# Kernel optimization log

Hardware: AMD Instinct MI355X
Metric: run time of the kernel (lower is better)

The kernel has to match this reference:

```python
import jax, jax.numpy as jnp
import numpy as np

T, D = 4096, 1024
S = 32768
DIST_DIM = 20
BINS = jnp.array([1, 2, 3, 4, 8, 16, 32, 64], dtype=jnp.int64)


def setup_inputs() -> dict:
    key = jax.random.key(0)
    ks = jax.random.split(key, 16)
    scale = 1.0 / np.sqrt(D)
    inp = {
        "embeds": jax.random.normal(ks[0], (T, D), dtype=jnp.float32),
        "states": jax.random.normal(ks[1], (T, D), dtype=jnp.float32),
        # MHA (1 head) projection params, torch Linear convention: x @ W.T + b
        "Wq": jax.random.normal(ks[2], (D, D), dtype=jnp.float32) * scale,
        "bq": jnp.zeros((D,), dtype=jnp.float32),
        "Wk": jax.random.normal(ks[3], (D, D), dtype=jnp.float32) * scale,
        "bk": jnp.zeros((D,), dtype=jnp.float32),
        "Wv": jax.random.normal(ks[4], (D, D), dtype=jnp.float32) * scale,
        "bv": jnp.zeros((D,), dtype=jnp.float32),
        "Wo": jax.random.normal(ks[5], (D, D), dtype=jnp.float32) * scale,
        "bo": jnp.zeros((D,), dtype=jnp.float32),
        # distance embedding table: len(bins)+1 = 9 rows
        "dist_embed": jax.random.normal(ks[6], (9, DIST_DIM), dtype=jnp.float32),
        "span_starts": jax.random.randint(ks[7], (S,), 0, T - 30, dtype=jnp.int64),
        "span_lengths": jax.random.randint(ks[8], (S,), 0, 30, dtype=jnp.int64),
    }
    return inp


def reference(embeds, states, Wq, bq, Wk, bk, Wv, bv, Wo, bo, dist_embed,
              span_starts, span_lengths):
    d = states.shape[1]
    # Single-head attention: query=states, key=states, value=embeds (seq len T, batch 1)
    q = states @ Wq.T + bq                      # [T, D]
    k = states @ Wk.T + bk                      # [T, D]
    v = embeds @ Wv.T + bv                      # [T, D]
    scores = (q @ k.T) / jnp.sqrt(jnp.asarray(d, q.dtype))   # [T, T]
    attn = jax.nn.softmax(scores, axis=-1)
    attn_embeds = (attn @ v) @ Wo.T + bo        # [T, D]

    ends = span_starts + span_lengths           # inclusive end, width 1..30
    # ragged per-span segment sum over [start, end] via prefix sums
    cs = jnp.concatenate([jnp.zeros((1, d), attn_embeds.dtype),
                          jnp.cumsum(attn_embeds, axis=0)], axis=0)  # [T+1, D]
    span_sum = cs[ends + 1] - cs[span_starts]   # [S, D]

    span_start_end = jnp.concatenate([states[span_starts], states[ends]], axis=1)  # [S, 2D]

    lengths = span_lengths + 1                  # len(span) = end - start + 1
    bin_idx = jnp.sum(lengths[:, None] > BINS[None, :], axis=-1)  # [S] in [0, 8]
    len_embed = dist_embed[bin_idx]             # [S, DIST_DIM] (dropout omitted: eval mode)

    return jnp.concatenate([span_sum, span_start_end, len_embed], axis=1)  # [S, 3D+20]
```

## Files before the change

### kernel.cpp

```cpp
#include <hip/hip_runtime.h>
#include <hip/hip_bf16.h>


typedef __attribute__((ext_vector_type(8))) short bf16x8;
typedef __attribute__((ext_vector_type(4))) short bf16x4;
typedef __attribute__((ext_vector_type(4))) float f32x4;

#define T_DIM 4096
#define D_DIM 1024
#define S_NUM 32768

#define GLOBAL_LOAD_LDS16(gptr, ldsptr)                                        \
  __builtin_amdgcn_global_load_lds(                                            \
      (const __attribute__((address_space(1))) void*)(gptr),                   \
      (__attribute__((address_space(3))) void*)(ldsptr), 16, 0, 0)

__global__ __launch_bounds__(256) void cast2_bf16(const float* __restrict__ a,
                                                  const float* __restrict__ b,
                                                  __hip_bfloat16* __restrict__ oa,
                                                  __hip_bfloat16* __restrict__ ob) {
  const float* s = blockIdx.z ? b : a;
  __hip_bfloat16* d = blockIdx.z ? ob : oa;
  int i = blockIdx.x * 256 + threadIdx.x;
  float2 v = ((const float2*)s)[i];
  __hip_bfloat162 o;
  o.x = __float2bfloat16(v.x);
  o.y = __float2bfloat16(v.y);
  ((__hip_bfloat162*)d)[i] = o;
}

__global__ __launch_bounds__(256) void cast3_bf16(const float* __restrict__ a,
                                                  const float* __restrict__ b,
                                                  const float* __restrict__ c,
                                                  __hip_bfloat16* __restrict__ oa,
                                                  __hip_bfloat16* __restrict__ ob,
                                                  __hip_bfloat16* __restrict__ oc) {
  const int z = blockIdx.z;
  const float* s = z == 0 ? a : z == 1 ? b : c;
  __hip_bfloat16* d = z == 0 ? oa : z == 1 ? ob : oc;
  int i = blockIdx.x * 256 + threadIdx.x;
  float2 v = ((const float2*)s)[i];
  __hip_bfloat162 o;
  o.x = __float2bfloat16(v.x);
  o.y = __float2bfloat16(v.y);
  ((__hip_bfloat162*)d)[i] = o;
}

__global__ __launch_bounds__(256) void transpose_cast_bf16(const float* __restrict__ in,
                                                           __hip_bfloat16* __restrict__ out) {
  __shared__ float tile[64][65];
  const int bx = blockIdx.x * 64;
  const int by = blockIdx.y * 64;
  const int t = threadIdx.x;
  const int r = t >> 4;
  const int c4 = (t & 15) * 4;
#pragma unroll
  for (int p = 0; p < 4; p++) {
    const float4 v = *(const float4*)&in[(size_t)(by + p * 16 + r) * D_DIM + bx + c4];
    tile[p * 16 + r][c4] = v.x;
    tile[p * 16 + r][c4 + 1] = v.y;
    tile[p * 16 + r][c4 + 2] = v.z;
    tile[p * 16 + r][c4 + 3] = v.w;
  }
  __syncthreads();
#pragma unroll
  for (int p = 0; p < 4; p++) {
    const int orow = p * 16 + r;
    bf16x4 o4;
#pragma unroll
    for (int q = 0; q < 4; q++) {
      __hip_bfloat16 h = __float2bfloat16(tile[c4 + q][orow]);
      o4[q] = *reinterpret_cast<short*>(&h);
    }
    *reinterpret_cast<bf16x4*>(&out[(size_t)(bx + orow) * D_DIM + by + c4]) = o4;
  }
}

__global__ __launch_bounds__(256) void zero_f32(float* __restrict__ p, int n) {
  int i = blockIdx.x * 256 + threadIdx.x;
  if (i < n) p[i] = 0.0f;
}

__global__ __launch_bounds__(256) void bias_fuse(const float* __restrict__ Wo,
                                                 const float* __restrict__ bv,
                                                 const float* __restrict__ bo,
                                                 float* __restrict__ bvo) {
  const int wave = threadIdx.x >> 6, lane = threadIdx.x & 63;
  const int row = blockIdx.x * 4 + wave;
  float s = 0.0f;
  for (int k = lane; k < D_DIM; k += 64) s += Wo[(size_t)row * D_DIM + k] * bv[k];
#pragma unroll
  for (int off = 32; off; off >>= 1) s += __shfl_xor(s, off);
  if (lane == 0) bvo[row] = s + bo[row];
}

__device__ __forceinline__ void gemm_core_128(const __hip_bfloat16* __restrict__ A,
                                              const __hip_bfloat16* __restrict__ B,
                                              int K, int lda, int ldb,
                                              int bm, int bn,
                                              __hip_bfloat16* As,
                                              __hip_bfloat16* Bs,
                                              f32x4 acc[4][4]) {
  const int tid = threadIdx.x;
  const int wave = tid >> 6, lane = tid & 63;
  const int srow = lane >> 2, scol = (lane & 3) * 8;
  const __hip_bfloat16* Ag0 = A + (size_t)(bm + wave * 16 + srow) * lda + scol;
  const __hip_bfloat16* Ag1 = Ag0 + (size_t)64 * lda;
  const __hip_bfloat16* Bg0 = B + (size_t)(bn + wave * 16 + srow) * ldb + scol;
  const __hip_bfloat16* Bg1 = Bg0 + (size_t)64 * ldb;
  const int c0 = wave * 512, c1 = (4 + wave) * 512;
  const int wtr = (wave >> 1) * 64, wtc = (wave & 1) * 64;
  const int lr = lane & 15, lk = (lane >> 4) * 8;

  GLOBAL_LOAD_LDS16(Ag0, As + c0);
  GLOBAL_LOAD_LDS16(Ag1, As + c1);
  GLOBAL_LOAD_LDS16(Bg0, Bs + c0);
  GLOBAL_LOAD_LDS16(Bg1, Bs + c1);

  int cur = 0;
  for (int k0 = 0; k0 < K; k0 += 32) {
    __syncthreads();
    const int nxt = cur ^ 1;
    if (k0 + 32 < K) {
      const int kn = k0 + 32;
      GLOBAL_LOAD_LDS16(Ag0 + kn, As + nxt * 4096 + c0);
      GLOBAL_LOAD_LDS16(Ag1 + kn, As + nxt * 4096 + c1);
      GLOBAL_LOAD_LDS16(Bg0 + kn, Bs + nxt * 4096 + c0);
      GLOBAL_LOAD_LDS16(Bg1 + kn, Bs + nxt * 4096 + c1);
    }
    const __hip_bfloat16* a = As + cur * 4096;
    const __hip_bfloat16* b = Bs + cur * 4096;
    bf16x8 af[4], bfr[4];
#pragma unroll
    for (int i = 0; i < 4; i++)
      af[i] = *(const bf16x8*)&a[(wtr + i * 16 + lr) * 32 + lk];
#pragma unroll
    for (int j = 0; j < 4; j++)
      bfr[j] = *(const bf16x8*)&b[(wtc + j * 16 + lr) * 32 + lk];
#pragma unroll
    for (int i = 0; i < 4; i++)
#pragma unroll
      for (int j = 0; j < 4; j++)
        acc[i][j] = __builtin_amdgcn_mfma_f32_16x16x32_bf16(af[i], bfr[j], acc[i][j], 0, 0, 0);
    cur = nxt;
  }
}


__global__ __launch_bounds__(256) void wvo_gemm_splitk(const __hip_bfloat16* __restrict__ Wo_bf,
                                                       const __hip_bfloat16* __restrict__ WvT_bf,
                                                       float* __restrict__ part) {
  __shared__ __hip_bfloat16 As[2 * 128 * 32];
  __shared__ __hip_bfloat16 Bs[2 * 128 * 32];
  const int z = blockIdx.z;
  const int bm = blockIdx.y * 128, bn = blockIdx.x * 128;
  const int wave = threadIdx.x >> 6, lane = threadIdx.x & 63;
  const int wtr = (wave >> 1) * 64, wtc = (wave & 1) * 64;
  const int lr = lane & 15;
  f32x4 acc[4][4] = {};
  gemm_core_128(Wo_bf + z * 256, WvT_bf + z * 256, 256, D_DIM, D_DIM, bm, bn, As, Bs, acc);
  float* dst = part + (size_t)z * D_DIM * D_DIM;
#pragma unroll
  for (int j = 0; j < 4; j++) {
    const int col = bn + wtc + j * 16 + lr;
#pragma unroll
    for (int i = 0; i < 4; i++)
#pragma unroll
      for (int r = 0; r < 4; r++) {
        const int row = bm + wtr + i * 16 + (lane >> 4) * 4 + r;
        dst[(size_t)row * D_DIM + col] = acc[i][j][r];
      }
  }
}

__global__ __launch_bounds__(256) void wvo_combine(const float* __restrict__ part,
                                                   __hip_bfloat16* __restrict__ out) {
  const size_t idx = (size_t)blockIdx.x * 256 + threadIdx.x;
  const size_t n = (size_t)D_DIM * D_DIM / 4;
  f32x4 s = ((const f32x4*)part)[idx];
  s += ((const f32x4*)part)[idx + n];
  s += ((const f32x4*)part)[idx + 2 * n];
  s += ((const f32x4*)part)[idx + 3 * n];
  bf16x4 o;
#pragma unroll
  for (int q = 0; q < 4; q++) {
    __hip_bfloat16 h = __float2bfloat16(s[q]);
    o[q] = *reinterpret_cast<short*>(&h);
  }
  ((bf16x4*)out)[idx] = o;
}

__global__ __launch_bounds__(256) void qkv_gemm(const __hip_bfloat16* __restrict__ states_bf,
                                                const __hip_bfloat16* __restrict__ embeds_bf,
                                                const __hip_bfloat16* __restrict__ Wq,
                                                const __hip_bfloat16* __restrict__ Wk,
                                                const __hip_bfloat16* __restrict__ Wvo,
                                                const float* __restrict__ bq,
                                                const float* __restrict__ bk,
                                                __hip_bfloat16* __restrict__ q,
                                                __hip_bfloat16* __restrict__ k,
                                                __hip_bfloat16* __restrict__ vT) {
  __shared__ __hip_bfloat16 As[2 * 128 * 32];
  __shared__ __hip_bfloat16 Bs[2 * 128 * 32];
  const int z = blockIdx.z;
  const __hip_bfloat16* A = (z == 2) ? embeds_bf : states_bf;
  const __hip_bfloat16* B = (z == 0) ? Wq : (z == 1) ? Wk : Wvo;
  const float* bias = (z == 0) ? bq : bk;
  const int bm = blockIdx.y * 128, bn = blockIdx.x * 128;
  const int wave = threadIdx.x >> 6, lane = threadIdx.x & 63;
  const int wtr = (wave >> 1) * 64, wtc = (wave & 1) * 64;
  const int lr = lane & 15;
  f32x4 acc[4][4] = {};
  gemm_core_128(A, B, D_DIM, D_DIM, D_DIM, bm, bn, As, Bs, acc);

#pragma unroll
  for (int j = 0; j < 4; j++) {
    const int col = bn + wtc + j * 16 + lr;
    const float bb = (z == 2) ? 0.0f : bias[col];
#pragma unroll
    for (int i = 0; i < 4; i++) {
#pragma unroll
      for (int r = 0; r < 4; r++) {
        const int row = bm + wtr + i * 16 + (lane >> 4) * 4 + r;
        const __hip_bfloat16 val = __float2bfloat16(acc[i][j][r] + bb);
        if (z == 0)
          q[(size_t)row * D_DIM + col] = val;
        else if (z == 1)
          k[(size_t)row * D_DIM + col] = val;
        else
          vT[(size_t)col * T_DIM + row] = val;
      }
    }
  }
}

__global__ __launch_bounds__(256) void scoresP_gemm(const __hip_bfloat16* __restrict__ q,
                                                    const __hip_bfloat16* __restrict__ k,
                                                    __hip_bfloat16* __restrict__ P,
                                                    float* __restrict__ l) {
  __shared__ __hip_bfloat16 As[2 * 128 * 32];
  __shared__ __hip_bfloat16 Bs[2 * 128 * 32];
  const int bm = blockIdx.y * 128, bn = blockIdx.x * 128;
  const int wave = threadIdx.x >> 6, lane = threadIdx.x & 63;
  const int wtr = (wave >> 1) * 64, wtc = (wave & 1) * 64;
  const int lr = lane & 15;
  f32x4 acc[4][4] = {};
  gemm_core_128(q, k, D_DIM, D_DIM, D_DIM, bm, bn, As, Bs, acc);

  float rowsum[4][4];
#pragma unroll
  for (int i = 0; i < 4; i++)
#pragma unroll
    for (int r = 0; r < 4; r++) rowsum[i][r] = 0.0f;

#pragma unroll
  for (int j = 0; j < 4; j++) {
    const int col = bn + wtc + j * 16 + lr;
#pragma unroll
    for (int i = 0; i < 4; i++) {
#pragma unroll
      for (int r = 0; r < 4; r++) {
        const int row = bm + wtr + i * 16 + (lane >> 4) * 4 + r;
        const float e = __expf(acc[i][j][r] * 0.03125f);
        P[(size_t)row * T_DIM + col] = __float2bfloat16(e);
        rowsum[i][r] += e;
      }
    }
  }
#pragma unroll
  for (int off = 1; off < 16; off <<= 1)
#pragma unroll
    for (int i = 0; i < 4; i++)
#pragma unroll
      for (int r = 0; r < 4; r++)
        rowsum[i][r] += __shfl_xor(rowsum[i][r], off);
  if ((lane & 15) == 0) {
#pragma unroll
    for (int i = 0; i < 4; i++)
#pragma unroll
      for (int r = 0; r < 4; r++) {
        const int row = bm + wtr + i * 16 + (lane >> 4) * 4 + r;
        atomicAdd(&l[row], rowsum[i][r]);
      }
  }
}

__global__ __launch_bounds__(256) void pv_gemm_splitk(const __hip_bfloat16* __restrict__ P,
                                                      const __hip_bfloat16* __restrict__ vT,
                                                      float* __restrict__ part) {
  __shared__ __hip_bfloat16 As[2 * 128 * 32];
  __shared__ __hip_bfloat16 Bs[2 * 128 * 32];
  const int z = blockIdx.z;
  const int bm = blockIdx.y * 128, bn = blockIdx.x * 128;
  const int wave = threadIdx.x >> 6, lane = threadIdx.x & 63;
  const int wtr = (wave >> 1) * 64, wtc = (wave & 1) * 64;
  const int lr = lane & 15;
  f32x4 acc[4][4] = {};
  gemm_core_128(P + z * 2048, vT + z * 2048, 2048, T_DIM, T_DIM, bm, bn, As, Bs, acc);
  float* dst = part + (size_t)z * T_DIM * D_DIM;
#pragma unroll
  for (int j = 0; j < 4; j++) {
    const int col = bn + wtc + j * 16 + lr;
#pragma unroll
    for (int i = 0; i < 4; i++)
#pragma unroll
      for (int r = 0; r < 4; r++) {
        const int row = bm + wtr + i * 16 + (lane >> 4) * 4 + r;
        dst[(size_t)row * D_DIM + col] = acc[i][j][r];
      }
  }
}

__global__ __launch_bounds__(256) void pv_combine(const float* __restrict__ part,
                                                  const float* __restrict__ l,
                                                  const float* __restrict__ bvo,
                                                  float* __restrict__ ao) {
  const size_t idx = (size_t)blockIdx.x * 256 + threadIdx.x;
  const size_t n = (size_t)T_DIM * D_DIM / 4;
  const int row = (int)(idx >> 8);
  const int c4 = (int)(idx & 255) * 4;
  const float inv = 1.0f / l[row];
  f32x4 a = ((const f32x4*)part)[idx];
  f32x4 b = ((const f32x4*)part)[idx + n];
  f32x4 bb = *(const f32x4*)(bvo + c4);
  f32x4 r = (a + b) * inv + bb;
  ((f32x4*)ao)[idx] = r;
}

__global__ __launch_bounds__(256) void colsum_chunks(const float* __restrict__ x,
                                                     float* __restrict__ part) {
  const int col = blockIdx.x * 256 + threadIdx.x;
  const int ch = blockIdx.y;
  const float* p = x + (size_t)ch * 64 * D_DIM + col;
  float s = 0.0f;
#pragma unroll 8
  for (int i = 0; i < 64; i++) s += p[i * D_DIM];
  part[ch * D_DIM + col] = s;
}

__global__ __launch_bounds__(256) void scan_chunks(float* part) {
  const int col = blockIdx.x * 256 + threadIdx.x;
  float run = 0.0f;
  for (int ch = 0; ch < 64; ch++) {
    const float t = part[ch * D_DIM + col];
    part[ch * D_DIM + col] = run;
    run += t;
  }
}

__global__ __launch_bounds__(256) void write_cs(const float* __restrict__ x,
                                                const float* __restrict__ part,
                                                float* __restrict__ cs) {
  const int col = blockIdx.x * 256 + threadIdx.x;
  const int ch = blockIdx.y;
  float run = part[ch * D_DIM + col];
  if (ch == 0) cs[col] = 0.0f;
  const float* p = x + (size_t)ch * 64 * D_DIM + col;
  float* q = cs + ((size_t)(ch * 64 + 1)) * D_DIM + col;
  for (int i = 0; i < 64; i++) {
    run += p[i * D_DIM];
    q[i * D_DIM] = run;
  }
}

__global__ __launch_bounds__(256) void hist_k(const int* __restrict__ starts,
                                              int* __restrict__ hist) {
  const int s = blockIdx.x * 256 + threadIdx.x;
  atomicAdd(&hist[starts[s]], 1);
}

__global__ __launch_bounds__(1024) void scan_hist(const int* __restrict__ hist,
                                                  int* __restrict__ offs) {
  __shared__ int sums[1024];
  const int t = threadIdx.x;
  const int v0 = hist[t * 4], v1 = hist[t * 4 + 1];
  const int v2 = hist[t * 4 + 2], v3 = hist[t * 4 + 3];
  const int tot = v0 + v1 + v2 + v3;
  sums[t] = tot;
  __syncthreads();
  for (int off = 1; off < 1024; off <<= 1) {
    const int x = (t >= off) ? sums[t - off] : 0;
    __syncthreads();
    sums[t] += x;
    __syncthreads();
  }
  const int excl = sums[t] - tot;
  offs[t * 4] = excl;
  offs[t * 4 + 1] = excl + v0;
  offs[t * 4 + 2] = excl + v0 + v1;
  offs[t * 4 + 3] = excl + v0 + v1 + v2;
}

__global__ __launch_bounds__(256) void scatter_k(const int* __restrict__ starts,
                                                 int* __restrict__ offs,
                                                 int* __restrict__ perm) {
  const int s = blockIdx.x * 256 + threadIdx.x;
  const int pos = atomicAdd(&offs[starts[s]], 1);
  perm[pos] = s;
}

__global__ __launch_bounds__(256) void span_gather(const float* __restrict__ cs,
                                                   const float* __restrict__ states,
                                                   const float* __restrict__ dist,
                                                   const int* __restrict__ starts,
                                                   const int* __restrict__ lens,
                                                   const int* __restrict__ perm,
                                                   float* __restrict__ out) {
  const int s = perm[blockIdx.x];
  const int start = starts[s];
  const int len = lens[s];
  const int end = start + len;
  const int length = len + 1;
  const int bin = (length > 1) + (length > 2) + (length > 3) + (length > 4) +
                  (length > 8) + (length > 16) + (length > 32) + (length > 64);
  const f32x4* csS = (const f32x4*)(cs + (size_t)start * D_DIM);
  const f32x4* csE = (const f32x4*)(cs + (size_t)(end + 1) * D_DIM);
  const f32x4* stS = (const f32x4*)(states + (size_t)start * D_DIM);
  const f32x4* stE = (const f32x4*)(states + (size_t)end * D_DIM);
  const f32x4* de = (const f32x4*)(dist + bin * 20);
  f32x4* o = (f32x4*)(out + (size_t)s * 3092);
  for (int j = threadIdx.x; j < 773; j += 256) {
    f32x4 r;
    if (j < 256) {
      r = csE[j] - csS[j];
    } else if (j < 512) {
      r = stS[j - 256];
    } else if (j < 768) {
      r = stE[j - 512];
    } else {
      r = de[j - 768];
    }
    __builtin_nontemporal_store(r, o + j);
  }
}

extern "C" void kernel_launch(void* const* d_in, const int* in_sizes, int n_in,
                              void* d_out, int out_size, void* d_ws, size_t ws_size,
                              hipStream_t stream) {
  const float* embeds = (const float*)d_in[0];
  const float* states = (const float*)d_in[1];
  const float* Wq = (const float*)d_in[2];
  const float* bq = (const float*)d_in[3];
  const float* Wk = (const float*)d_in[4];
  const float* bk = (const float*)d_in[5];
  const float* Wv = (const float*)d_in[6];
  const float* bv = (const float*)d_in[7];
  const float* Wo = (const float*)d_in[8];
  const float* bo = (const float*)d_in[9];
  const float* dist = (const float*)d_in[10];
  const int* starts = (const int*)d_in[11];
  const int* lens = (const int*)d_in[12];
  float* out = (float*)d_out;

  const size_t TD = (size_t)T_DIM * D_DIM;
  const size_t DD = (size_t)D_DIM * D_DIM;
  const size_t TT = (size_t)T_DIM * T_DIM;

  char* w = (char*)d_ws;
  size_t off = 0;
  auto alloc = [&](size_t bytes) {
    char* p = w + off;
    off = (off + bytes + 255) & ~(size_t)255;
    return p;
  };
  __hip_bfloat16* states_bf = (__hip_bfloat16*)alloc(TD * 2);
  __hip_bfloat16* embeds_bf = (__hip_bfloat16*)alloc(TD * 2);
  __hip_bfloat16* Wq_bf = (__hip_bfloat16*)alloc(DD * 2);
  __hip_bfloat16* Wk_bf = (__hip_bfloat16*)alloc(DD * 2);
  __hip_bfloat16* Wo_bf = (__hip_bfloat16*)alloc(DD * 2);
  __hip_bfloat16* WvT_bf = (__hip_bfloat16*)alloc(DD * 2);
  __hip_bfloat16* Wvo_bf = (__hip_bfloat16*)alloc(DD * 2);
  __hip_bfloat16* q_bf = (__hip_bfloat16*)alloc(TD * 2);
  __hip_bfloat16* k_bf = (__hip_bfloat16*)alloc(TD * 2);
  __hip_bfloat16* vT_bf = (__hip_bfloat16*)alloc(TD * 2);
  __hip_bfloat16* P_bf = (__hip_bfloat16*)alloc(TT * 2);
  float* l_sum = (float*)alloc(T_DIM * 4);
  int* hist = (int*)alloc(T_DIM * 4);
  int* offs = (int*)alloc(T_DIM * 4);
  int* perm = (int*)alloc(S_NUM * 4);
  float* bvo = (float*)alloc(D_DIM * 4);
  float* ao = (float*)alloc(TD * 4);
  float* cs = (float*)alloc((size_t)(T_DIM + 1) * D_DIM * 4);
  float* part = (float*)alloc(64 * D_DIM * 4);
  float* wvo_part = (float*)alloc(4 * DD * 4);
  float* pv_part = (float*)alloc(2 * TD * 4);
  if (off > ws_size) return;

  cast2_bf16<<<dim3(TD / 512, 1, 2), 256, 0, stream>>>(states, embeds, states_bf, embeds_bf);
  cast3_bf16<<<dim3(DD / 512, 1, 3), 256, 0, stream>>>(Wq, Wk, Wo, Wq_bf, Wk_bf, Wo_bf);
  transpose_cast_bf16<<<dim3(16, 16), 256, 0, stream>>>(Wv, WvT_bf);
  zero_f32<<<2 * T_DIM / 256, 256, 0, stream>>>(l_sum, 2 * T_DIM);
  bias_fuse<<<D_DIM / 4, 256, 0, stream>>>(Wo, bv, bo, bvo);

  hist_k<<<S_NUM / 256, 256, 0, stream>>>(starts, hist);
  scan_hist<<<1, 1024, 0, stream>>>(hist, offs);
  scatter_k<<<S_NUM / 256, 256, 0, stream>>>(starts, offs, perm);

  wvo_gemm_splitk<<<dim3(D_DIM / 128, D_DIM / 128, 4), 256, 0, stream>>>(Wo_bf, WvT_bf, wvo_part);
  wvo_combine<<<DD / 1024, 256, 0, stream>>>(wvo_part, Wvo_bf);

  qkv_gemm<<<dim3(D_DIM / 128, T_DIM / 128, 3), 256, 0, stream>>>(
      states_bf, embeds_bf, Wq_bf, Wk_bf, Wvo_bf, bq, bk, q_bf, k_bf, vT_bf);

  scoresP_gemm<<<dim3(T_DIM / 128, T_DIM / 128), 256, 0, stream>>>(q_bf, k_bf, P_bf, l_sum);

  pv_gemm_splitk<<<dim3(D_DIM / 128, T_DIM / 128, 2), 256, 0, stream>>>(P_bf, vT_bf, pv_part);
  pv_combine<<<TD / 1024, 256, 0, stream>>>(pv_part, l_sum, bvo, ao);

  colsum_chunks<<<dim3(4, 64), 256, 0, stream>>>(ao, part);
  scan_chunks<<<4, 256, 0, stream>>>(part);
  write_cs<<<dim3(4, 64), 256, 0, stream>>>(ao, part, cs);

  span_gather<<<S_NUM, 256, 0, stream>>>(cs, states, dist, starts, lens, perm, out);
}
```

Measured before the change: 712.0 us.

## Fold Wq·Wk into one weight product and fuse PV combine with column sums

Scores are rewritten as states·(Wq^T Wk)·states^T plus bias-derived row and column vectors. The Q and K projection GEMMs (two T×D×D) become one small D×D×D weight GEMM plus one T×D×D projection GEMM, so projection work is roughly halved. The PV combine is also fused with the per-chunk column sums, and the separate chunk-scan kernel is removed. Each write_cs block now rescans the partial sums itself. Precision differs because the combined weight M1 is rounded to bf16 and the raw states replace the rounded q and k.

```diff
diff --git a/kernel.cpp b/kernel.cpp
--- a/kernel.cpp
+++ b/kernel.cpp
@@ -29,26 +29,26 @@
   ((__hip_bfloat162*)d)[i] = o;
 }
 
-__global__ __launch_bounds__(256) void cast3_bf16(const float* __restrict__ a,
-                                                  const float* __restrict__ b,
-                                                  const float* __restrict__ c,
-                                                  __hip_bfloat16* __restrict__ oa,
-                                                  __hip_bfloat16* __restrict__ ob,
-                                                  __hip_bfloat16* __restrict__ oc) {
-  const int z = blockIdx.z;
-  const float* s = z == 0 ? a : z == 1 ? b : c;
-  __hip_bfloat16* d = z == 0 ? oa : z == 1 ? ob : oc;
+__global__ __launch_bounds__(256) void cast1_bf16(const float* __restrict__ a,
+                                                  __hip_bfloat16* __restrict__ oa) {
   int i = blockIdx.x * 256 + threadIdx.x;
-  float2 v = ((const float2*)s)[i];
+  float2 v = ((const float2*)a)[i];
   __hip_bfloat162 o;
   o.x = __float2bfloat16(v.x);
   o.y = __float2bfloat16(v.y);
-  ((__hip_bfloat162*)d)[i] = o;
-}
-
-__global__ __launch_bounds__(256) void transpose_cast_bf16(const float* __restrict__ in,
-                                                           __hip_bfloat16* __restrict__ out) {
+  ((__hip_bfloat162*)oa)[i] = o;
+}
+
+__global__ __launch_bounds__(256) void transpose_cast_bf16(const float* __restrict__ wq,
+                                                           const float* __restrict__ wk,
+                                                           const float* __restrict__ wv,
+                                                           __hip_bfloat16* __restrict__ oq,
+                                                           __hip_bfloat16* __restrict__ ok,
+                                                           __hip_bfloat16* __restrict__ ov) {
   __shared__ float tile[64][65];
+  const int z = blockIdx.z;
+  const float* in = z == 0 ? wq : z == 1 ? wk : wv;
+  __hip_bfloat16* out = z == 0 ? oq : z == 1 ? ok : ov;
   const int bx = blockIdx.x * 64;
   const int by = blockIdx.y * 64;
   const int t = threadIdx.x;
@@ -81,17 +81,61 @@
   if (i < n) p[i] = 0.0f;
 }
 
-__global__ __launch_bounds__(256) void bias_fuse(const float* __restrict__ Wo,
-                                                 const float* __restrict__ bv,
-                                                 const float* __restrict__ bo,
-                                                 float* __restrict__ bvo) {
+__global__ __launch_bounds__(256) void hvec(const float* __restrict__ Wo,
+                                            const float* __restrict__ bv,
+                                            const float* __restrict__ bo,
+                                            const __hip_bfloat16* __restrict__ WqT,
+                                            const __hip_bfloat16* __restrict__ WkT,
+                                            const float* __restrict__ bq,
+                                            const float* __restrict__ bk,
+                                            float* __restrict__ bvo,
+                                            float* __restrict__ h1,
+                                            float* __restrict__ h2,
+                                            float* __restrict__ c0) {
+  const int z = blockIdx.z;
   const int wave = threadIdx.x >> 6, lane = threadIdx.x & 63;
   const int row = blockIdx.x * 4 + wave;
+  if (z == 3 && (blockIdx.x != 0 || wave != 0)) return;
   float s = 0.0f;
-  for (int k = lane; k < D_DIM; k += 64) s += Wo[(size_t)row * D_DIM + k] * bv[k];
+  if (z == 0) {
+    for (int k2 = lane; k2 < D_DIM; k2 += 64) s += Wo[(size_t)row * D_DIM + k2] * bv[k2];
+  } else if (z == 1) {
+    for (int k2 = lane; k2 < D_DIM; k2 += 64)
+      s += __bfloat162float(WqT[(size_t)row * D_DIM + k2]) * bk[k2];
+  } else if (z == 2) {
+    for (int k2 = lane; k2 < D_DIM; k2 += 64)
+      s += __bfloat162float(WkT[(size_t)row * D_DIM + k2]) * bq[k2];
+  } else {
+    for (int k2 = lane; k2 < D_DIM; k2 += 64) s += bq[k2] * bk[k2];
+  }
 #pragma unroll
   for (int off = 32; off; off >>= 1) s += __shfl_xor(s, off);
-  if (lane == 0) bvo[row] = s + bo[row];
+  if (lane == 0) {
+    if (z == 0) bvo[row] = s + bo[row];
+    else if (z == 1) h1[row] = s;
+    else if (z == 2) h2[row] = s;
+    else c0[0] = s;
+  }
+}
+
+__global__ __launch_bounds__(256) void uw_vec(const float* __restrict__ states,
+                                              const float* __restrict__ h1,
+                                              const float* __restrict__ h2,
+                                              const float* __restrict__ c0,
+                                              float* __restrict__ u,
+                                              float* __restrict__ w) {
+  const int z = blockIdx.z;
+  const int wave = threadIdx.x >> 6, lane = threadIdx.x & 63;
+  const int row = blockIdx.x * 4 + wave;
+  const float* h = z == 0 ? h1 : h2;
+  float s = 0.0f;
+  for (int k2 = lane; k2 < D_DIM; k2 += 64) s += states[(size_t)row * D_DIM + k2] * h[k2];
+#pragma unroll
+  for (int off = 32; off; off >>= 1) s += __shfl_xor(s, off);
+  if (lane == 0) {
+    if (z == 0) u[row] = s + c0[0];
+    else w[row] = s;
+  }
 }
 
 __device__ __forceinline__ void gemm_core_128(const __hip_bfloat16* __restrict__ A,
@@ -147,18 +191,23 @@
 }
 
 
-__global__ __launch_bounds__(256) void wvo_gemm_splitk(const __hip_bfloat16* __restrict__ Wo_bf,
-                                                       const __hip_bfloat16* __restrict__ WvT_bf,
-                                                       float* __restrict__ part) {
+__global__ __launch_bounds__(256) void small_gemm_splitk(const __hip_bfloat16* __restrict__ Wo_bf,
+                                                         const __hip_bfloat16* __restrict__ WvT_bf,
+                                                         const __hip_bfloat16* __restrict__ WkT_bf,
+                                                         const __hip_bfloat16* __restrict__ WqT_bf,
+                                                         float* __restrict__ part) {
   __shared__ __hip_bfloat16 As[2 * 128 * 32];
   __shared__ __hip_bfloat16 Bs[2 * 128 * 32];
   const int z = blockIdx.z;
+  const int zz = z & 3;
+  const __hip_bfloat16* A = (z < 4) ? Wo_bf + zz * 256 : WkT_bf + zz * 256;
+  const __hip_bfloat16* B = (z < 4) ? WvT_bf + zz * 256 : WqT_bf + zz * 256;
   const int bm = blockIdx.y * 128, bn = blockIdx.x * 128;
   const int wave = threadIdx.x >> 6, lane = threadIdx.x & 63;
   const int wtr = (wave >> 1) * 64, wtc = (wave & 1) * 64;
   const int lr = lane & 15;
   f32x4 acc[4][4] = {};
-  gemm_core_128(Wo_bf + z * 256, WvT_bf + z * 256, 256, D_DIM, D_DIM, bm, bn, As, Bs, acc);
+  gemm_core_128(A, B, 256, D_DIM, D_DIM, bm, bn, As, Bs, acc);
   float* dst = part + (size_t)z * D_DIM * D_DIM;
 #pragma unroll
   for (int j = 0; j < 4; j++) {
@@ -173,39 +222,34 @@
   }
 }
 
-__global__ __launch_bounds__(256) void wvo_combine(const float* __restrict__ part,
-                                                   __hip_bfloat16* __restrict__ out) {
+__global__ __launch_bounds__(256) void small_combine(const float* __restrict__ part,
+                                                     __hip_bfloat16* __restrict__ wvo,
+                                                     __hip_bfloat16* __restrict__ m1) {
   const size_t idx = (size_t)blockIdx.x * 256 + threadIdx.x;
   const size_t n = (size_t)D_DIM * D_DIM / 4;
-  f32x4 s = ((const f32x4*)part)[idx];
-  s += ((const f32x4*)part)[idx + n];
-  s += ((const f32x4*)part)[idx + 2 * n];
-  s += ((const f32x4*)part)[idx + 3 * n];
+  const f32x4* base = (const f32x4*)part + (size_t)blockIdx.z * 4 * n;
+  f32x4 s = base[idx] + base[idx + n] + base[idx + 2 * n] + base[idx + 3 * n];
   bf16x4 o;
 #pragma unroll
   for (int q = 0; q < 4; q++) {
     __hip_bfloat16 h = __float2bfloat16(s[q]);
     o[q] = *reinterpret_cast<short*>(&h);
   }
+  __hip_bfloat16* out = blockIdx.z == 0 ? wvo : m1;
   ((bf16x4*)out)[idx] = o;
 }
 
-__global__ __launch_bounds__(256) void qkv_gemm(const __hip_bfloat16* __restrict__ states_bf,
-                                                const __hip_bfloat16* __restrict__ embeds_bf,
-                                                const __hip_bfloat16* __restrict__ Wq,
-                                                const __hip_bfloat16* __restrict__ Wk,
-                                                const __hip_bfloat16* __restrict__ Wvo,
-                                                const float* __restrict__ bq,
-                                                const float* __restrict__ bk,
-                                                __hip_bfloat16* __restrict__ q,
-                                                __hip_bfloat16* __restrict__ k,
-                                                __hip_bfloat16* __restrict__ vT) {
+__global__ __launch_bounds__(256) void proj_gemm(const __hip_bfloat16* __restrict__ states_bf,
+                                                 const __hip_bfloat16* __restrict__ embeds_bf,
+                                                 const __hip_bfloat16* __restrict__ M1,
+                                                 const __hip_bfloat16* __restrict__ Wvo,
+                                                 __hip_bfloat16* __restrict__ tmp,
+                                                 __hip_bfloat16* __restrict__ vT) {
   __shared__ __hip_bfloat16 As[2 * 128 * 32];
   __shared__ __hip_bfloat16 Bs[2 * 128 * 32];
   const int z = blockIdx.z;
-  const __hip_bfloat16* A = (z == 2) ? embeds_bf : states_bf;
-  const __hip_bfloat16* B = (z == 0) ? Wq : (z == 1) ? Wk : Wvo;
-  const float* bias = (z == 0) ? bq : bk;
+  const __hip_bfloat16* A = (z == 0) ? states_bf : embeds_bf;
+  const __hip_bfloat16* B = (z == 0) ? M1 : Wvo;
   const int bm = blockIdx.y * 128, bn = blockIdx.x * 128;
   const int wave = threadIdx.x >> 6, lane = threadIdx.x & 63;
   const int wtr = (wave >> 1) * 64, wtc = (wave & 1) * 64;
@@ -216,17 +260,14 @@
 #pragma unroll
   for (int j = 0; j < 4; j++) {
     const int col = bn + wtc + j * 16 + lr;
-    const float bb = (z == 2) ? 0.0f : bias[col];
 #pragma unroll
     for (int i = 0; i < 4; i++) {
 #pragma unroll
       for (int r = 0; r < 4; r++) {
         const int row = bm + wtr + i * 16 + (lane >> 4) * 4 + r;
-        const __hip_bfloat16 val = __float2bfloat16(acc[i][j][r] + bb);
+        const __hip_bfloat16 val = __float2bfloat16(acc[i][j][r]);
         if (z == 0)
-          q[(size_t)row * D_DIM + col] = val;
-        else if (z == 1)
-          k[(size_t)row * D_DIM + col] = val;
+          tmp[(size_t)row * D_DIM + col] = val;
         else
           vT[(size_t)col * T_DIM + row] = val;
       }
@@ -234,8 +275,10 @@
   }
 }
 
-__global__ __launch_bounds__(256) void scoresP_gemm(const __hip_bfloat16* __restrict__ q,
-                                                    const __hip_bfloat16* __restrict__ k,
+__global__ __launch_bounds__(256) void scoresP_gemm(const __hip_bfloat16* __restrict__ tmp,
+                                                    const __hip_bfloat16* __restrict__ states_bf,
+                                                    const float* __restrict__ u,
+                                                    const float* __restrict__ w,
                                                     __hip_bfloat16* __restrict__ P,
                                                     float* __restrict__ l) {
   __shared__ __hip_bfloat16 As[2 * 128 * 32];
@@ -245,7 +288,7 @@
   const int wtr = (wave >> 1) * 64, wtc = (wave & 1) * 64;
   const int lr = lane & 15;
   f32x4 acc[4][4] = {};
-  gemm_core_128(q, k, D_DIM, D_DIM, D_DIM, bm, bn, As, Bs, acc);
+  gemm_core_128(tmp, states_bf, D_DIM, D_DIM, D_DIM, bm, bn, As, Bs, acc);
 
   float rowsum[4][4];
 #pragma unroll
@@ -256,12 +299,13 @@
 #pragma unroll
   for (int j = 0; j < 4; j++) {
     const int col = bn + wtc + j * 16 + lr;
+    const float ww = w[col];
 #pragma unroll
     for (int i = 0; i < 4; i++) {
 #pragma unroll
       for (int r = 0; r < 4; r++) {
         const int row = bm + wtr + i * 16 + (lane >> 4) * 4 + r;
-        const float e = __expf(acc[i][j][r] * 0.03125f);
+        const float e = __expf((acc[i][j][r] + u[row] + ww) * 0.03125f);
         P[(size_t)row * T_DIM + col] = __float2bfloat16(e);
         rowsum[i][r] += e;
       }
@@ -311,49 +355,34 @@
   }
 }
 
-__global__ __launch_bounds__(256) void pv_combine(const float* __restrict__ part,
-                                                  const float* __restrict__ l,
-                                                  const float* __restrict__ bvo,
-                                                  float* __restrict__ ao) {
-  const size_t idx = (size_t)blockIdx.x * 256 + threadIdx.x;
-  const size_t n = (size_t)T_DIM * D_DIM / 4;
-  const int row = (int)(idx >> 8);
-  const int c4 = (int)(idx & 255) * 4;
-  const float inv = 1.0f / l[row];
-  f32x4 a = ((const f32x4*)part)[idx];
-  f32x4 b = ((const f32x4*)part)[idx + n];
-  f32x4 bb = *(const f32x4*)(bvo + c4);
-  f32x4 r = (a + b) * inv + bb;
-  ((f32x4*)ao)[idx] = r;
-}
-
-__global__ __launch_bounds__(256) void colsum_chunks(const float* __restrict__ x,
-                                                     float* __restrict__ part) {
+__global__ __launch_bounds__(256) void pv_combine_colsum(const float* __restrict__ part,
+                                                         const float* __restrict__ l,
+                                                         const float* __restrict__ bvo,
+                                                         float* __restrict__ ao,
+                                                         float* __restrict__ partT) {
   const int col = blockIdx.x * 256 + threadIdx.x;
   const int ch = blockIdx.y;
-  const float* p = x + (size_t)ch * 64 * D_DIM + col;
+  const size_t n = (size_t)T_DIM * D_DIM;
+  const float bb = bvo[col];
   float s = 0.0f;
-#pragma unroll 8
-  for (int i = 0; i < 64; i++) s += p[i * D_DIM];
-  part[ch * D_DIM + col] = s;
-}
-
-__global__ __launch_bounds__(256) void scan_chunks(float* part) {
-  const int col = blockIdx.x * 256 + threadIdx.x;
-  float run = 0.0f;
-  for (int ch = 0; ch < 64; ch++) {
-    const float t = part[ch * D_DIM + col];
-    part[ch * D_DIM + col] = run;
-    run += t;
-  }
+  for (int i = 0; i < 64; i++) {
+    const int row = ch * 64 + i;
+    const float inv = 1.0f / l[row];
+    const size_t idx = (size_t)row * D_DIM + col;
+    const float v = (part[idx] + part[n + idx]) * inv + bb;
+    ao[idx] = v;
+    s += v;
+  }
+  partT[(col << 6) | ch] = s;
 }
 
 __global__ __launch_bounds__(256) void write_cs(const float* __restrict__ x,
-                                                const float* __restrict__ part,
+                                                const float* __restrict__ partT,
                                                 float* __restrict__ cs) {
   const int col = blockIdx.x * 256 + threadIdx.x;
   const int ch = blockIdx.y;
-  float run = part[ch * D_DIM + col];
+  float run = 0.0f;
+  for (int c = 0; c < ch; c++) run += partT[(col << 6) | c];
   if (ch == 0) cs[col] = 0.0f;
   const float* p = x + (size_t)ch * 64 * D_DIM + col;
   float* q = cs + ((size_t)(ch * 64 + 1)) * D_DIM + col;
@@ -465,13 +494,13 @@
   };
   __hip_bfloat16* states_bf = (__hip_bfloat16*)alloc(TD * 2);
   __hip_bfloat16* embeds_bf = (__hip_bfloat16*)alloc(TD * 2);
-  __hip_bfloat16* Wq_bf = (__hip_bfloat16*)alloc(DD * 2);
-  __hip_bfloat16* Wk_bf = (__hip_bfloat16*)alloc(DD * 2);
   __hip_bfloat16* Wo_bf = (__hip_bfloat16*)alloc(DD * 2);
+  __hip_bfloat16* WqT_bf = (__hip_bfloat16*)alloc(DD * 2);
+  __hip_bfloat16* WkT_bf = (__hip_bfloat16*)alloc(DD * 2);
   __hip_bfloat16* WvT_bf = (__hip_bfloat16*)alloc(DD * 2);
   __hip_bfloat16* Wvo_bf = (__hip_bfloat16*)alloc(DD * 2);
-  __hip_bfloat16* q_bf = (__hip_bfloat16*)alloc(TD * 2);
-  __hip_bfloat16* k_bf = (__hip_bfloat16*)alloc(TD * 2);
+  __hip_bfloat16* M1_bf = (__hip_bfloat16*)alloc(DD * 2);
+  __hip_bfloat16* tmp_bf = (__hip_bfloat16*)alloc(TD * 2);
   __hip_bfloat16* vT_bf = (__hip_bfloat16*)alloc(TD * 2);
   __hip_bfloat16* P_bf = (__hip_bfloat16*)alloc(TT * 2);
   float* l_sum = (float*)alloc(T_DIM * 4);
@@ -479,37 +508,45 @@
   int* offs = (int*)alloc(T_DIM * 4);
   int* perm = (int*)alloc(S_NUM * 4);
   float* bvo = (float*)alloc(D_DIM * 4);
+  float* h1 = (float*)alloc(D_DIM * 4);
+  float* h2 = (float*)alloc(D_DIM * 4);
+  float* c0 = (float*)alloc(256);
+  float* u = (float*)alloc(T_DIM * 4);
+  float* wv_ = (float*)alloc(T_DIM * 4);
   float* ao = (float*)alloc(TD * 4);
   float* cs = (float*)alloc((size_t)(T_DIM + 1) * D_DIM * 4);
-  float* part = (float*)alloc(64 * D_DIM * 4);
-  float* wvo_part = (float*)alloc(4 * DD * 4);
+  float* partT = (float*)alloc(64 * D_DIM * 4);
+  float* wpart = (float*)alloc(8 * DD * 4);
   float* pv_part = (float*)alloc(2 * TD * 4);
   if (off > ws_size) return;
 
   cast2_bf16<<<dim3(TD / 512, 1, 2), 256, 0, stream>>>(states, embeds, states_bf, embeds_bf);
-  cast3_bf16<<<dim3(DD / 512, 1, 3), 256, 0, stream>>>(Wq, Wk, Wo, Wq_bf, Wk_bf, Wo_bf);
-  transpose_cast_bf16<<<dim3(16, 16), 256, 0, stream>>>(Wv, WvT_bf);
+  cast1_bf16<<<DD / 512, 256, 0, stream>>>(Wo, Wo_bf);
+  transpose_cast_bf16<<<dim3(16, 16, 3), 256, 0, stream>>>(Wq, Wk, Wv, WqT_bf, WkT_bf, WvT_bf);
   zero_f32<<<2 * T_DIM / 256, 256, 0, stream>>>(l_sum, 2 * T_DIM);
-  bias_fuse<<<D_DIM / 4, 256, 0, stream>>>(Wo, bv, bo, bvo);
+  hvec<<<dim3(D_DIM / 4, 1, 4), 256, 0, stream>>>(Wo, bv, bo, WqT_bf, WkT_bf, bq, bk,
+                                                  bvo, h1, h2, c0);
 
   hist_k<<<S_NUM / 256, 256, 0, stream>>>(starts, hist);
   scan_hist<<<1, 1024, 0, stream>>>(hist, offs);
   scatter_k<<<S_NUM / 256, 256, 0, stream>>>(starts, offs, perm);
 
-  wvo_gemm_splitk<<<dim3(D_DIM / 128, D_DIM / 128, 4), 256, 0, stream>>>(Wo_bf, WvT_bf, wvo_part);
-  wvo_combine<<<DD / 1024, 256, 0, stream>>>(wvo_part, Wvo_bf);
-
-  qkv_gemm<<<dim3(D_DIM / 128, T_DIM / 128, 3), 256, 0, stream>>>(
-      states_bf, embeds_bf, Wq_bf, Wk_bf, Wvo_bf, bq, bk, q_bf, k_bf, vT_bf);
-
-  scoresP_gemm<<<dim3(T_DIM / 128, T_DIM / 128), 256, 0, stream>>>(q_bf, k_bf, P_bf, l_sum);
+  uw_vec<<<dim3(T_DIM / 4, 1, 2), 256, 0, stream>>>(states, h1, h2, c0, u, wv_);
+
+  small_gemm_splitk<<<dim3(D_DIM / 128, D_DIM / 128, 8), 256, 0, stream>>>(
+      Wo_bf, WvT_bf, WkT_bf, WqT_bf, wpart);
+  small_combine<<<dim3(DD / 1024, 1, 2), 256, 0, stream>>>(wpart, Wvo_bf, M1_bf);
+
+  proj_gemm<<<dim3(D_DIM / 128, T_DIM / 128, 2), 256, 0, stream>>>(
+      states_bf, embeds_bf, M1_bf, Wvo_bf, tmp_bf, vT_bf);
+
+  scoresP_gemm<<<dim3(T_DIM / 128, T_DIM / 128), 256, 0, stream>>>(
+      tmp_bf, states_bf, u, wv_, P_bf, l_sum);
 
   pv_gemm_splitk<<<dim3(D_DIM / 128, T_DIM / 128, 2), 256, 0, stream>>>(P_bf, vT_bf, pv_part);
-  pv_combine<<<TD / 1024, 256, 0, stream>>>(pv_part, l_sum, bvo, ao);
-
-  colsum_chunks<<<dim3(4, 64), 256, 0, stream>>>(ao, part);
-  scan_chunks<<<4, 256, 0, stream>>>(part);
-  write_cs<<<dim3(4, 64), 256, 0, stream>>>(ao, part, cs);
+  pv_combine_colsum<<<dim3(4, 64), 256, 0, stream>>>(pv_part, l_sum, bvo, ao, partT);
+
+  write_cs<<<dim3(4, 64), 256, 0, stream>>>(ao, partT, cs);
 
   span_gather<<<S_NUM, 256, 0, stream>>>(cs, states, dist, starts, lens, perm, out);
 }
```

Result: no change. 725.9 us (+1.9%).
